# Performance work log

Hardware: AMD Instinct MI355X
Metric: run time of the kernel (lower is better)

## Reference

```python
import jax, jax.numpy as jnp
import numpy as np

DIM = 2048
K_DIM = 2048
Q_HEADS = 16
KV_HEADS = 4
HEAD_DIM = DIM // Q_HEADS  # 128
KV_DIM = HEAD_DIM * KV_HEADS  # 512
MAX_LEN = 2048
ROPE_THETA = 10000.0
ROPE_FACTOR = 8.0


def _rope_cos_sin(seq_len):
    # Faithful to generate_sin_cos_pos_emb with is_causal=True
    d = HEAD_DIM
    seq_eff = max(seq_len, MAX_LEN)
    base_adj = (ROPE_FACTOR * seq_eff / MAX_LEN - (ROPE_FACTOR - 1.0)) ** (d / (d - 2))
    adjusted_base = ROPE_THETA * base_adj
    inv_freq = 1.0 / adjusted_base ** (np.arange(0, d, 2, dtype=np.float32) / d)
    pos = np.arange(seq_len, dtype=np.float32)  # causal: no centering
    freqs = pos[:, None] * inv_freq[None, :]            # [S, d/2]
    emb = np.concatenate([freqs, freqs], axis=-1)        # [S, d]
    return jnp.asarray(np.cos(emb), jnp.float32), jnp.asarray(np.sin(emb), jnp.float32)


def _rotate_half(x):
    x1, x2 = jnp.split(x, 2, axis=-1)
    return jnp.concatenate([-x2, x1], axis=-1)


def setup_inputs() -> dict:
    key = jax.random.key(0)
    ks = jax.random.split(key, 12)
    B, S = 1, 2048
    s_in = 1.0 / np.sqrt(DIM)
    s_k = 1.0 / np.sqrt(K_DIM)
    return {
        "query": jax.random.normal(ks[0], (B, S, DIM), jnp.float32),
        "key": jax.random.normal(ks[1], (B, S, K_DIM), jnp.float32),
        "value": jax.random.normal(ks[2], (B, S, K_DIM), jnp.float32),
        "Wq": jax.random.uniform(ks[3], (DIM, DIM), jnp.float32, -s_in, s_in),
        "bq": jax.random.uniform(ks[4], (DIM,), jnp.float32, -s_in, s_in),
        "Wk": jax.random.uniform(ks[5], (KV_DIM, K_DIM), jnp.float32, -s_k, s_k),
        "bk": jax.random.uniform(ks[6], (KV_DIM,), jnp.float32, -s_k, s_k),
        "Wv": jax.random.uniform(ks[7], (KV_DIM, K_DIM), jnp.float32, -s_k, s_k),
        "bv": jax.random.uniform(ks[8], (KV_DIM,), jnp.float32, -s_k, s_k),
        "Wo": jax.random.uniform(ks[9], (DIM, DIM), jnp.float32, -s_in, s_in),
        "bo": jax.random.uniform(ks[10], (DIM,), jnp.float32, -s_in, s_in),
    }


def reference(query, key, value, Wq, bq, Wk, bk, Wv, bv, Wo, bo):
    B, S, _ = query.shape
    scale = HEAD_DIM ** -0.5

    q = query @ Wq.T + bq                                   # [B,S,DIM]
    k = key @ Wk.T + bk                                     # [B,S,KV_DIM]
    v = value @ Wv.T + bv                                   # [B,S,KV_DIM]

    q = q.reshape(B, S, Q_HEADS, HEAD_DIM)
    k = k.reshape(B, S, KV_HEADS, HEAD_DIM)
    v = v.reshape(B, S, KV_HEADS, HEAD_DIM)

    cos, sin = _rope_cos_sin(S)                              # [S,D]
    cos = cos[None, :, None, :]
    sin = sin[None, :, None, :]
    q = q * cos + _rotate_half(q) * sin
    k = k * cos + _rotate_half(k) * sin

    # [B,H,S,D]
    q = q.transpose(0, 2, 1, 3)
    k = k.transpose(0, 2, 1, 3)
    v = v.transpose(0, 2, 1, 3)

    rep = Q_HEADS // KV_HEADS
    k = jnp.repeat(k, rep, axis=1)
    v = jnp.repeat(v, rep, axis=1)

    scores = jnp.einsum('bhqd,bhkd->bhqk', q, k) * scale
    causal = jnp.tril(jnp.ones((S, S), bool))
    scores = jnp.where(causal[None, None], scores, jnp.finfo(scores.dtype).min)
    attn = jax.nn.softmax(scores, axis=-1)
    out = jnp.einsum('bhqk,bhkd->bhqd', attn, v)             # [B,H,S,D]

    out = out.transpose(0, 2, 1, 3).reshape(B, S, DIM)
    return out @ Wo.T + bo
```

## Files before the change

### kernel.cpp

```cpp
#include <hip/hip_runtime.h>
#include <stdint.h>

typedef __attribute__((ext_vector_type(8))) short short8;
typedef __attribute__((ext_vector_type(4))) float f32x4;
typedef __attribute__((ext_vector_type(4))) unsigned short u16x4;
typedef unsigned short bf16_t;

__device__ __forceinline__ bf16_t f2bf(float f) {
  union { float f; uint32_t u; } x; x.f = f;
  uint32_t r = x.u + 0x7fffu + ((x.u >> 16) & 1u);
  return (bf16_t)(r >> 16);
}

__device__ __forceinline__ void ld_g2l_16(const bf16_t* g, bf16_t* l) {
  __builtin_amdgcn_global_load_lds(
      (const __attribute__((address_space(1))) void*)g,
      (__attribute__((address_space(3))) void*)l, 16, 0, 0);
}

__global__ void rope_tab(float* __restrict__ CS, float* __restrict__ SN) {
  int idx = blockIdx.x * 256 + threadIdx.x;
  int i = idx & 63, pos = idx >> 6;
  float ang = (float)pos * exp2f((float)i * -0.2076205059f);
  CS[idx] = cosf(ang);
  SN[idx] = sinf(ang);
}

__global__ void convert_all(const float* __restrict__ s0, const float* __restrict__ s1,
                            const float* __restrict__ s2, const float* __restrict__ s3,
                            const float* __restrict__ s4, const float* __restrict__ s5,
                            const float* __restrict__ s6,
                            bf16_t* __restrict__ d0, bf16_t* __restrict__ d1,
                            bf16_t* __restrict__ d2, bf16_t* __restrict__ d3,
                            bf16_t* __restrict__ d4, bf16_t* __restrict__ d5,
                            bf16_t* __restrict__ d6) {
  int i = blockIdx.x * 256 + threadIdx.x;
  const float* src; bf16_t* dst; int off;
  if (i < 5 * 1048576) {
    int t = i >> 20; off = i & 1048575;
    if (t == 0)      { src = s0; dst = d0; }
    else if (t == 1) { src = s1; dst = d1; }
    else if (t == 2) { src = s2; dst = d2; }
    else if (t == 3) { src = s3; dst = d3; }
    else             { src = s4; dst = d4; }
  } else {
    int j = i - 5 * 1048576;
    if (j < 262144) { src = s5; dst = d5; off = j; }
    else            { src = s6; dst = d6; off = j - 262144; }
  }
  f32x4 v = *(const f32x4*)(src + (size_t)off * 4);
  u16x4 o;
  o[0] = f2bf(v[0]); o[1] = f2bf(v[1]); o[2] = f2bf(v[2]); o[3] = f2bf(v[3]);
  *(u16x4*)(dst + (size_t)off * 4) = o;
}

template <int MODE>
__device__ __forceinline__ void gemm_core(
    bf16_t* __restrict__ As, bf16_t* __restrict__ Bs,
    const bf16_t* __restrict__ A, const bf16_t* __restrict__ Bm,
    const float* __restrict__ bias, void* __restrict__ Cout,
    int N, int K, int m0, int n0,
    const float* __restrict__ CS, const float* __restrict__ SN) {
  const int tid = threadIdx.x;
  const int lane = tid & 63, quad = lane >> 4, l16 = lane & 15;
  const int wv = tid >> 6;
  const int wr = wv >> 1, wc = wv & 1;

  f32x4 acc[2][4];
  const f32x4 zf = {0.f, 0.f, 0.f, 0.f};
#pragma unroll
  for (int mi = 0; mi < 2; ++mi)
#pragma unroll
    for (int ni = 0; ni < 4; ++ni) acc[mi][ni] = zf;

  const int rA = tid >> 2, cA = (tid & 3) * 8;
  const bf16_t* Ap  = A + (size_t)(m0 + rA) * K + cA;
  const bf16_t* Bp0 = Bm + (size_t)(n0 + rA) * K + cA;
  const bf16_t* Bp1 = Bm + (size_t)(n0 + 64 + rA) * K + cA;
  bf16_t* lA  = As + tid * 8;
  bf16_t* lB0 = Bs + tid * 8;
  bf16_t* lB1 = Bs + (tid + 256) * 8;

  for (int k0 = 0; k0 < K; k0 += 32) {
    ld_g2l_16(Ap + k0, lA);
    ld_g2l_16(Bp0 + k0, lB0);
    ld_g2l_16(Bp1 + k0, lB1);
    __syncthreads();
    short8 af[2], bf[4];
#pragma unroll
    for (int mi = 0; mi < 2; ++mi)
      af[mi] = *(const short8*)(&As[(wr * 32 + mi * 16 + l16) * 32 + quad * 8]);
#pragma unroll
    for (int ni = 0; ni < 4; ++ni)
      bf[ni] = *(const short8*)(
          &Bs[(wc * 32 + (ni & 1) * 16 + (ni >> 1) * 64 + l16) * 32 + quad * 8]);
#pragma unroll
    for (int mi = 0; mi < 2; ++mi)
#pragma unroll
      for (int ni = 0; ni < 4; ++ni)
        acc[mi][ni] = __builtin_amdgcn_mfma_f32_16x16x32_bf16(
            af[mi], bf[ni], acc[mi][ni], 0, 0, 0);
    __syncthreads();
  }

  if (MODE == 0 || MODE == 2) {
#pragma unroll
    for (int mi = 0; mi < 2; ++mi)
#pragma unroll
      for (int ni = 0; ni < 4; ++ni) {
        int n = n0 + wc * 32 + (ni & 1) * 16 + (ni >> 1) * 64 + l16;
        int mbase = m0 + wr * 32 + mi * 16 + quad * 4;
        float bv = bias[n];
#pragma unroll
        for (int r = 0; r < 4; ++r) {
          float v = acc[mi][ni][r] + bv;
          int m = mbase + r;
          if (MODE == 0) ((float*)Cout)[(size_t)m * N + n] = v;
          else           ((bf16_t*)Cout)[(size_t)n * 2048 + m] = f2bf(v);
        }
      }
  } else {
    const float scale = (MODE == 3) ? 0.12751744f : 1.0f;
    bf16_t* dst = (bf16_t*)Cout;
#pragma unroll
    for (int mi = 0; mi < 2; ++mi)
#pragma unroll
      for (int r = 0; r < 4; ++r) {
        int m = m0 + wr * 32 + mi * 16 + quad * 4 + r;
#pragma unroll
        for (int ni = 0; ni < 2; ++ni) {
          int i = wc * 32 + ni * 16 + l16;
          int n_lo = n0 + i;
          float v1 = acc[mi][ni][r] + bias[n_lo];
          float v2 = acc[mi][ni + 2][r] + bias[n_lo + 64];
          float c = CS[m * 64 + i];
          float s = SN[m * 64 + i];
          float o1 = (v1 * c - v2 * s) * scale;
          float o2 = (v2 * c + v1 * s) * scale;
          dst[(size_t)m * N + n_lo] = f2bf(o1);
          dst[(size_t)m * N + n_lo + 64] = f2bf(o2);
        }
      }
  }
}

__global__ __launch_bounds__(256) void gemm_qkv(
    const bf16_t* __restrict__ qb, const bf16_t* __restrict__ kb,
    const bf16_t* __restrict__ vb, const bf16_t* __restrict__ wqb,
    const bf16_t* __restrict__ wkb, const bf16_t* __restrict__ wvb,
    const float* __restrict__ bq, const float* __restrict__ bk,
    const float* __restrict__ bv, bf16_t* __restrict__ Qr,
    bf16_t* __restrict__ Kr, bf16_t* __restrict__ Vt,
    const float* __restrict__ CS, const float* __restrict__ SN) {
  __shared__ __align__(16) bf16_t As[64 * 32];
  __shared__ __align__(16) bf16_t Bs[128 * 32];
  int bx = blockIdx.x, m0 = blockIdx.y * 64;
  if (bx < 16)
    gemm_core<3>(As, Bs, qb, wqb, bq, Qr, 2048, 2048, m0, bx * 128, CS, SN);
  else if (bx < 20)
    gemm_core<4>(As, Bs, kb, wkb, bk, Kr, 512, 2048, m0, (bx - 16) * 128, CS, SN);
  else
    gemm_core<2>(As, Bs, vb, wvb, bv, Vt, 512, 2048, m0, (bx - 20) * 128, CS, SN);
}

__global__ __launch_bounds__(256) void gemm_o(
    const bf16_t* __restrict__ Ob, const bf16_t* __restrict__ wob,
    const float* __restrict__ bo, float* __restrict__ out) {
  __shared__ __align__(16) bf16_t As[64 * 32];
  __shared__ __align__(16) bf16_t Bs[128 * 32];
  gemm_core<0>(As, Bs, Ob, wob, bo, out, 2048, 2048,
               blockIdx.y * 64, blockIdx.x * 128, nullptr, nullptr);
}

__global__ __launch_bounds__(256, 2) void attn_fwd(
    const bf16_t* __restrict__ Qr, const bf16_t* __restrict__ Kr,
    const bf16_t* __restrict__ Vt, bf16_t* __restrict__ Oo) {
  const int h = blockIdx.y;
  const int bx = blockIdx.x;
  const int qt = (h < 8) ? (31 - bx) : bx;
  const int T = qt + 1;

  const int tid = threadIdx.x;
  const int wv = tid >> 6, lane = tid & 63, quad = lane >> 4, l16 = lane & 15;
  const int q_base = qt * 64 + wv * 16;
  const int hkv = h >> 2;
  const int qg = q_base + l16;
  const int swzE = (l16 & 7) << 3;

  __shared__ __align__(16) bf16_t Ks[2][64 * 128];
  __shared__ __align__(16) bf16_t Vs[2][128 * 64];

  short8 qf[4];
  {
    const bf16_t* qp = Qr + (size_t)qg * 2048 + h * 128 + quad * 8;
#pragma unroll
    for (int kc = 0; kc < 4; ++kc) qf[kc] = *(const short8*)(qp + kc * 32);
  }

  const f32x4 zf = {0.f, 0.f, 0.f, 0.f};
  f32x4 o[8];
#pragma unroll
  for (int di = 0; di < 8; ++di) o[di] = zf;
  float l_acc = 0.f;

  auto STAGE = [&](int buf, int t) {
    const int k0 = t * 64;
    bf16_t* KB = &Ks[buf][0];
    bf16_t* VB = &Vs[buf][0];
#pragma unroll
    for (int m = 0; m < 4; ++m) {
      int rK = wv * 16 + m * 4 + (lane >> 4);
      const bf16_t* gK = Kr + (size_t)(k0 + rK) * 512 + hkv * 128
                         + (((lane & 15) ^ ((4 * (m & 1)) | quad)) << 3);
      ld_g2l_16(gK, KB + rK * 128 + ((lane & 15) << 3));
      int rV = wv * 32 + m * 8 + (lane >> 3);
      const bf16_t* gV = Vt + (size_t)(hkv * 128 + rV) * 2048 + k0
                         + (((lane & 7) ^ ((lane >> 3) & 7)) << 3);
      ld_g2l_16(gV, VB + rV * 64 + ((lane & 7) << 3));
    }
  };

  STAGE(0, 0);
  __syncthreads();
  int buf = 0;

  for (int t = 0; t < T; ++t) {
    if (t + 1 < T) STAGE(buf ^ 1, t + 1);
    const bf16_t* KB = &Ks[buf][0];
    const bf16_t* VB = &Vs[buf][0];
    const int k0 = t * 64;

    f32x4 sacc[4];
#pragma unroll
    for (int sub = 0; sub < 4; ++sub) sacc[sub] = zf;
#pragma unroll
    for (int sub = 0; sub < 4; ++sub)
#pragma unroll
      for (int kc = 0; kc < 4; ++kc) {
        short8 kf = *(const short8*)(
            &KB[(sub * 16 + l16) * 128 + ((kc * 32 + quad * 8) ^ swzE)]);
        sacc[sub] = __builtin_amdgcn_mfma_f32_16x16x32_bf16(kf, qf[kc], sacc[sub], 0, 0, 0);
      }

    const bool dg = (k0 + 63 > q_base);
    uint32_t Dw[4][2];
#pragma unroll
    for (int sub = 0; sub < 4; ++sub) {
      float pv[4];
#pragma unroll
      for (int r = 0; r < 4; ++r) {
        float e = exp2f(sacc[sub][r]);
        if (dg) {
          int kg = k0 + sub * 16 + quad * 4 + r;
          if (kg > qg) e = 0.f;
        }
        pv[r] = e;
        l_acc += e;
      }
      asm("v_cvt_pk_bf16_f32 %0, %1, %2" : "=v"(Dw[sub][0]) : "v"(pv[0]), "v"(pv[1]));
      asm("v_cvt_pk_bf16_f32 %0, %1, %2" : "=v"(Dw[sub][1]) : "v"(pv[2]), "v"(pv[3]));
    }

    const int aA = ((((quad * 2) & 3) << 4) + l16) << 2;
    const int aB = ((((quad * 2 + 1) & 3) << 4) + l16) << 2;
    const bool losel = quad < 2;
#define BPERM(a, x) ((uint32_t)__builtin_amdgcn_ds_bpermute((a), (int)(x)))
    union { uint32_t w[4]; short8 v; } U0, U1;
    {
      uint32_t t0, t1;
      t0 = BPERM(aA, Dw[0][0]); t1 = BPERM(aA, Dw[1][0]); U0.w[0] = losel ? t0 : t1;
      t0 = BPERM(aA, Dw[0][1]); t1 = BPERM(aA, Dw[1][1]); U0.w[1] = losel ? t0 : t1;
      t0 = BPERM(aB, Dw[0][0]); t1 = BPERM(aB, Dw[1][0]); U0.w[2] = losel ? t0 : t1;
      t0 = BPERM(aB, Dw[0][1]); t1 = BPERM(aB, Dw[1][1]); U0.w[3] = losel ? t0 : t1;
      t0 = BPERM(aA, Dw[2][0]); t1 = BPERM(aA, Dw[3][0]); U1.w[0] = losel ? t0 : t1;
      t0 = BPERM(aA, Dw[2][1]); t1 = BPERM(aA, Dw[3][1]); U1.w[1] = losel ? t0 : t1;
      t0 = BPERM(aB, Dw[2][0]); t1 = BPERM(aB, Dw[3][0]); U1.w[2] = losel ? t0 : t1;
      t0 = BPERM(aB, Dw[2][1]); t1 = BPERM(aB, Dw[3][1]); U1.w[3] = losel ? t0 : t1;
    }
#undef BPERM
    const short8 pf0 = U0.v, pf1 = U1.v;

#pragma unroll
    for (int di = 0; di < 8; ++di) {
      short8 vf0 = *(const short8*)(
          &VB[(di * 16 + l16) * 64 + ((quad * 8) ^ swzE)]);
      short8 vf1 = *(const short8*)(
          &VB[(di * 16 + l16) * 64 + ((quad * 8 + 32) ^ swzE)]);
      o[di] = __builtin_amdgcn_mfma_f32_16x16x32_bf16(pf0, vf0, o[di], 0, 0, 0);
      o[di] = __builtin_amdgcn_mfma_f32_16x16x32_bf16(pf1, vf1, o[di], 0, 0, 0);
    }

    __asm__ volatile("s_waitcnt vmcnt(0)" ::: "memory");
    __syncthreads();
    buf ^= 1;
  }

  float lf = l_acc;
  lf += __shfl_xor(lf, 16);
  lf += __shfl_xor(lf, 32);
  float linv[4];
#pragma unroll
  for (int r = 0; r < 4; ++r) linv[r] = 1.0f / __shfl(lf, quad * 4 + r, 64);
#pragma unroll
  for (int di = 0; di < 8; ++di)
#pragma unroll
    for (int r = 0; r < 4; ++r) {
      size_t row = q_base + quad * 4 + r;
      size_t col = h * 128 + di * 16 + l16;
      Oo[row * 2048 + col] = f2bf(o[di][r] * linv[r]);
    }
}

extern "C" void kernel_launch(void* const* d_in, const int* in_sizes, int n_in,
                              void* d_out, int out_size, void* d_ws, size_t ws_size,
                              hipStream_t stream) {
  (void)in_sizes; (void)n_in; (void)out_size; (void)ws_size;
  const float* query = (const float*)d_in[0];
  const float* key = (const float*)d_in[1];
  const float* value = (const float*)d_in[2];
  const float* Wq = (const float*)d_in[3];
  const float* bq = (const float*)d_in[4];
  const float* Wk = (const float*)d_in[5];
  const float* bk = (const float*)d_in[6];
  const float* Wv = (const float*)d_in[7];
  const float* bv = (const float*)d_in[8];
  const float* Wo = (const float*)d_in[9];
  const float* bo = (const float*)d_in[10];
  float* out = (float*)d_out;

  char* ws = (char*)d_ws;
  const size_t MB = 1024 * 1024;
  bf16_t* qb  = (bf16_t*)(ws + 0 * MB);
  bf16_t* kb  = (bf16_t*)(ws + 8 * MB);
  bf16_t* vb  = (bf16_t*)(ws + 16 * MB);
  bf16_t* wqb = (bf16_t*)(ws + 24 * MB);
  bf16_t* wkb = (bf16_t*)(ws + 32 * MB);
  bf16_t* wvb = (bf16_t*)(ws + 34 * MB);
  bf16_t* wob = (bf16_t*)(ws + 36 * MB);
  bf16_t* Qr  = (bf16_t*)(ws + 44 * MB);
  bf16_t* Kr  = (bf16_t*)(ws + 52 * MB);
  bf16_t* Vt  = (bf16_t*)(ws + 54 * MB);
  bf16_t* Ob  = (bf16_t*)(ws + 56 * MB);
  float*  CS  = (float*)(ws + 64 * MB);
  float*  SN  = (float*)(ws + 64 * MB + 512 * 1024);

  rope_tab<<<512, 256, 0, stream>>>(CS, SN);
  convert_all<<<22528, 256, 0, stream>>>(query, key, value, Wq, Wo, Wk, Wv,
                                         qb, kb, vb, wqb, wob, wkb, wvb);
  gemm_qkv<<<dim3(24, 32), 256, 0, stream>>>(qb, kb, vb, wqb, wkb, wvb,
                                             bq, bk, bv, Qr, Kr, Vt, CS, SN);
  attn_fwd<<<dim3(32, 16), 256, 0, stream>>>(Qr, Kr, Vt, Ob);
  gemm_o<<<dim3(16, 32), 256, 0, stream>>>(Ob, wob, bo, out);
}
```

Measured before the change: 273.5 us.

## Fuse all stages into one persistent megakernel with grid-wide atomic barriers

```diff
diff --git a/kernel.cpp b/kernel.cpp
--- a/kernel.cpp
+++ b/kernel.cpp
@@ -18,41 +18,24 @@
       (__attribute__((address_space(3))) void*)l, 16, 0, 0);
 }
 
-__global__ void rope_tab(float* __restrict__ CS, float* __restrict__ SN) {
-  int idx = blockIdx.x * 256 + threadIdx.x;
-  int i = idx & 63, pos = idx >> 6;
-  float ang = (float)pos * exp2f((float)i * -0.2076205059f);
-  CS[idx] = cosf(ang);
-  SN[idx] = sinf(ang);
-}
-
-__global__ void convert_all(const float* __restrict__ s0, const float* __restrict__ s1,
-                            const float* __restrict__ s2, const float* __restrict__ s3,
-                            const float* __restrict__ s4, const float* __restrict__ s5,
-                            const float* __restrict__ s6,
-                            bf16_t* __restrict__ d0, bf16_t* __restrict__ d1,
-                            bf16_t* __restrict__ d2, bf16_t* __restrict__ d3,
-                            bf16_t* __restrict__ d4, bf16_t* __restrict__ d5,
-                            bf16_t* __restrict__ d6) {
-  int i = blockIdx.x * 256 + threadIdx.x;
-  const float* src; bf16_t* dst; int off;
-  if (i < 5 * 1048576) {
-    int t = i >> 20; off = i & 1048575;
-    if (t == 0)      { src = s0; dst = d0; }
-    else if (t == 1) { src = s1; dst = d1; }
-    else if (t == 2) { src = s2; dst = d2; }
-    else if (t == 3) { src = s3; dst = d3; }
-    else             { src = s4; dst = d4; }
-  } else {
-    int j = i - 5 * 1048576;
-    if (j < 262144) { src = s5; dst = d5; off = j; }
-    else            { src = s6; dst = d6; off = j - 262144; }
-  }
-  f32x4 v = *(const f32x4*)(src + (size_t)off * 4);
-  u16x4 o;
-  o[0] = f2bf(v[0]); o[1] = f2bf(v[1]); o[2] = f2bf(v[2]); o[3] = f2bf(v[3]);
-  *(u16x4*)(dst + (size_t)off * 4) = o;
-}
+__device__ __forceinline__ void gsync(unsigned* bar, unsigned target) {
+  __syncthreads();
+  if (threadIdx.x == 0) {
+    __threadfence();
+    atomicAdd(bar, 1u);
+    while (__hip_atomic_load(bar, __ATOMIC_ACQUIRE,
+                             __HIP_MEMORY_SCOPE_AGENT) < target) {}
+    __threadfence();
+  }
+  __syncthreads();
+}
+
+struct MegaArgs {
+  const float *query, *key, *value;
+  const float *Wq, *bq, *Wk, *bk, *Wv, *bv, *Wo, *bo;
+  float* out;
+  char* ws;
+};
 
 template <int MODE>
 __device__ __forceinline__ void gemm_core(
@@ -144,39 +127,11 @@
   }
 }
 
-__global__ __launch_bounds__(256) void gemm_qkv(
-    const bf16_t* __restrict__ qb, const bf16_t* __restrict__ kb,
-    const bf16_t* __restrict__ vb, const bf16_t* __restrict__ wqb,
-    const bf16_t* __restrict__ wkb, const bf16_t* __restrict__ wvb,
-    const float* __restrict__ bq, const float* __restrict__ bk,
-    const float* __restrict__ bv, bf16_t* __restrict__ Qr,
-    bf16_t* __restrict__ Kr, bf16_t* __restrict__ Vt,
-    const float* __restrict__ CS, const float* __restrict__ SN) {
-  __shared__ __align__(16) bf16_t As[64 * 32];
-  __shared__ __align__(16) bf16_t Bs[128 * 32];
-  int bx = blockIdx.x, m0 = blockIdx.y * 64;
-  if (bx < 16)
-    gemm_core<3>(As, Bs, qb, wqb, bq, Qr, 2048, 2048, m0, bx * 128, CS, SN);
-  else if (bx < 20)
-    gemm_core<4>(As, Bs, kb, wkb, bk, Kr, 512, 2048, m0, (bx - 16) * 128, CS, SN);
-  else
-    gemm_core<2>(As, Bs, vb, wvb, bv, Vt, 512, 2048, m0, (bx - 20) * 128, CS, SN);
-}
-
-__global__ __launch_bounds__(256) void gemm_o(
-    const bf16_t* __restrict__ Ob, const bf16_t* __restrict__ wob,
-    const float* __restrict__ bo, float* __restrict__ out) {
-  __shared__ __align__(16) bf16_t As[64 * 32];
-  __shared__ __align__(16) bf16_t Bs[128 * 32];
-  gemm_core<0>(As, Bs, Ob, wob, bo, out, 2048, 2048,
-               blockIdx.y * 64, blockIdx.x * 128, nullptr, nullptr);
-}
-
-__global__ __launch_bounds__(256, 2) void attn_fwd(
-    const bf16_t* __restrict__ Qr, const bf16_t* __restrict__ Kr,
-    const bf16_t* __restrict__ Vt, bf16_t* __restrict__ Oo) {
-  const int h = blockIdx.y;
-  const int bx = blockIdx.x;
+__device__ __forceinline__ void attn_block(
+    int b, const bf16_t* __restrict__ Qr, const bf16_t* __restrict__ Kr,
+    const bf16_t* __restrict__ Vt, bf16_t* __restrict__ Oo, char* smem) {
+  const int h = b >> 5;
+  const int bx = b & 31;
   const int qt = (h < 8) ? (31 - bx) : bx;
   const int T = qt + 1;
 
@@ -187,9 +142,6 @@
   const int qg = q_base + l16;
   const int swzE = (l16 & 7) << 3;
 
-  __shared__ __align__(16) bf16_t Ks[2][64 * 128];
-  __shared__ __align__(16) bf16_t Vs[2][128 * 64];
-
   short8 qf[4];
   {
     const bf16_t* qp = Qr + (size_t)qg * 2048 + h * 128 + quad * 8;
@@ -205,8 +157,8 @@
 
   auto STAGE = [&](int buf, int t) {
     const int k0 = t * 64;
-    bf16_t* KB = &Ks[buf][0];
-    bf16_t* VB = &Vs[buf][0];
+    bf16_t* KB = (bf16_t*)(smem + buf * 16384);
+    bf16_t* VB = (bf16_t*)(smem + 32768 + buf * 16384);
 #pragma unroll
     for (int m = 0; m < 4; ++m) {
       int rK = wv * 16 + m * 4 + (lane >> 4);
@@ -226,8 +178,8 @@
 
   for (int t = 0; t < T; ++t) {
     if (t + 1 < T) STAGE(buf ^ 1, t + 1);
-    const bf16_t* KB = &Ks[buf][0];
-    const bf16_t* VB = &Vs[buf][0];
+    const bf16_t* KB = (const bf16_t*)(smem + buf * 16384);
+    const bf16_t* VB = (const bf16_t*)(smem + 32768 + buf * 16384);
     const int k0 = t * 64;
 
     f32x4 sacc[4];
@@ -311,24 +263,9 @@
     }
 }
 
-extern "C" void kernel_launch(void* const* d_in, const int* in_sizes, int n_in,
-                              void* d_out, int out_size, void* d_ws, size_t ws_size,
-                              hipStream_t stream) {
-  (void)in_sizes; (void)n_in; (void)out_size; (void)ws_size;
-  const float* query = (const float*)d_in[0];
-  const float* key = (const float*)d_in[1];
-  const float* value = (const float*)d_in[2];
-  const float* Wq = (const float*)d_in[3];
-  const float* bq = (const float*)d_in[4];
-  const float* Wk = (const float*)d_in[5];
-  const float* bk = (const float*)d_in[6];
-  const float* Wv = (const float*)d_in[7];
-  const float* bv = (const float*)d_in[8];
-  const float* Wo = (const float*)d_in[9];
-  const float* bo = (const float*)d_in[10];
-  float* out = (float*)d_out;
-
-  char* ws = (char*)d_ws;
+__global__ __launch_bounds__(256, 2) void mega(MegaArgs a) {
+  __shared__ __align__(16) char smem[65536];
+  char* ws = a.ws;
   const size_t MB = 1024 * 1024;
   bf16_t* qb  = (bf16_t*)(ws + 0 * MB);
   bf16_t* kb  = (bf16_t*)(ws + 8 * MB);
@@ -343,12 +280,83 @@
   bf16_t* Ob  = (bf16_t*)(ws + 56 * MB);
   float*  CS  = (float*)(ws + 64 * MB);
   float*  SN  = (float*)(ws + 64 * MB + 512 * 1024);
-
-  rope_tab<<<512, 256, 0, stream>>>(CS, SN);
-  convert_all<<<22528, 256, 0, stream>>>(query, key, value, Wq, Wo, Wk, Wv,
-                                         qb, kb, vb, wqb, wob, wkb, wvb);
-  gemm_qkv<<<dim3(24, 32), 256, 0, stream>>>(qb, kb, vb, wqb, wkb, wvb,
-                                             bq, bk, bv, Qr, Kr, Vt, CS, SN);
-  attn_fwd<<<dim3(32, 16), 256, 0, stream>>>(Qr, Kr, Vt, Ob);
-  gemm_o<<<dim3(16, 32), 256, 0, stream>>>(Ob, wob, bo, out);
-}
+  unsigned* bar = (unsigned*)(ws + 65 * MB);
+
+  const int b = blockIdx.x, tid = threadIdx.x;
+
+  {
+    int idx = b * 256 + tid;
+    int fi = idx & 63, pos = idx >> 6;
+    float ang = (float)pos * exp2f((float)fi * -0.2076205059f);
+    CS[idx] = cosf(ang);
+    SN[idx] = sinf(ang);
+    for (int i = idx; i < 5767168; i += 131072) {
+      const float* src; bf16_t* dst; int off;
+      if (i < 5242880) {
+        int t = i >> 20; off = i & 1048575;
+        if (t == 0)      { src = a.query; dst = qb; }
+        else if (t == 1) { src = a.key;   dst = kb; }
+        else if (t == 2) { src = a.value; dst = vb; }
+        else if (t == 3) { src = a.Wq;    dst = wqb; }
+        else             { src = a.Wo;    dst = wob; }
+      } else {
+        int j = i - 5242880;
+        if (j < 262144) { src = a.Wk; dst = wkb; off = j; }
+        else            { src = a.Wv; dst = wvb; off = j - 262144; }
+      }
+      f32x4 v = *(const f32x4*)(src + (size_t)off * 4);
+      u16x4 o4;
+      o4[0] = f2bf(v[0]); o4[1] = f2bf(v[1]); o4[2] = f2bf(v[2]); o4[3] = f2bf(v[3]);
+      *(u16x4*)(dst + (size_t)off * 4) = o4;
+    }
+  }
+  gsync(&bar[0], 512);
+
+  {
+    bf16_t* As = (bf16_t*)smem;
+    bf16_t* Bs = (bf16_t*)(smem + 4096);
+    int j = b;
+    for (int rnd = 0; rnd < 2; ++rnd) {
+      int bx = j % 24, m0 = (j / 24) * 64;
+      if (bx < 16)
+        gemm_core<3>(As, Bs, qb, wqb, a.bq, Qr, 2048, 2048, m0, bx * 128, CS, SN);
+      else if (bx < 20)
+        gemm_core<4>(As, Bs, kb, wkb, a.bk, Kr, 512, 2048, m0, (bx - 16) * 128, CS, SN);
+      else
+        gemm_core<2>(As, Bs, vb, wvb, a.bv, Vt, 512, 2048, m0, (bx - 20) * 128, CS, SN);
+      if ((b & 1) != 0 || rnd == 1) break;
+      j = 512 + (b >> 1);
+      __syncthreads();
+    }
+  }
+  gsync(&bar[1], 512);
+
+  attn_block(b, Qr, Kr, Vt, Ob, smem);
+  gsync(&bar[2], 512);
+
+  {
+    bf16_t* As = (bf16_t*)smem;
+    bf16_t* Bs = (bf16_t*)(smem + 4096);
+    gemm_core<0>(As, Bs, Ob, wob, a.bo, a.out, 2048, 2048,
+                 (b >> 4) * 64, (b & 15) * 128, nullptr, nullptr);
+  }
+}
+
+extern "C" void kernel_launch(void* const* d_in, const int* in_sizes, int n_in,
+                              void* d_out, int out_size, void* d_ws, size_t ws_size,
+                              hipStream_t stream) {
+  (void)in_sizes; (void)n_in; (void)out_size; (void)ws_size;
+  MegaArgs a;
+  a.query = (const float*)d_in[0];
+  a.key   = (const float*)d_in[1];
+  a.value = (const float*)d_in[2];
+  a.Wq = (const float*)d_in[3];  a.bq = (const float*)d_in[4];
+  a.Wk = (const float*)d_in[5];  a.bk = (const float*)d_in[6];
+  a.Wv = (const float*)d_in[7];  a.bv = (const float*)d_in[8];
+  a.Wo = (const float*)d_in[9];  a.bo = (const float*)d_in[10];
+  a.out = (float*)d_out;
+  a.ws = (char*)d_ws;
+
+  hipMemsetAsync(a.ws + 65 * 1024 * 1024, 0, 256, stream);
+  mega<<<dim3(512), dim3(256), 0, stream>>>(a);
+}
```

Result: slower. 578.4 us (+111.5%).

## Load V fragments directly into registers and fold RoPE table into convert

Applied to the files above, without the earlier changes.

```diff
diff --git a/kernel.cpp b/kernel.cpp
--- a/kernel.cpp
+++ b/kernel.cpp
@@ -16,14 +16,6 @@
   __builtin_amdgcn_global_load_lds(
       (const __attribute__((address_space(1))) void*)g,
       (__attribute__((address_space(3))) void*)l, 16, 0, 0);
-}
-
-__global__ void rope_tab(float* __restrict__ CS, float* __restrict__ SN) {
-  int idx = blockIdx.x * 256 + threadIdx.x;
-  int i = idx & 63, pos = idx >> 6;
-  float ang = (float)pos * exp2f((float)i * -0.2076205059f);
-  CS[idx] = cosf(ang);
-  SN[idx] = sinf(ang);
 }
 
 __global__ void convert_all(const float* __restrict__ s0, const float* __restrict__ s1,
@@ -33,8 +25,15 @@
                             bf16_t* __restrict__ d0, bf16_t* __restrict__ d1,
                             bf16_t* __restrict__ d2, bf16_t* __restrict__ d3,
                             bf16_t* __restrict__ d4, bf16_t* __restrict__ d5,
-                            bf16_t* __restrict__ d6) {
+                            bf16_t* __restrict__ d6,
+                            float* __restrict__ CS, float* __restrict__ SN) {
   int i = blockIdx.x * 256 + threadIdx.x;
+  if (i < 131072) {
+    int fi = i & 63, pos = i >> 6;
+    float ang = (float)pos * exp2f((float)fi * -0.2076205059f);
+    CS[i] = cosf(ang);
+    SN[i] = sinf(ang);
+  }
   const float* src; bf16_t* dst; int off;
   if (i < 5 * 1048576) {
     int t = i >> 20; off = i & 1048575;
@@ -188,7 +187,6 @@
   const int swzE = (l16 & 7) << 3;
 
   __shared__ __align__(16) bf16_t Ks[2][64 * 128];
-  __shared__ __align__(16) bf16_t Vs[2][128 * 64];
 
   short8 qf[4];
   {
@@ -197,37 +195,43 @@
     for (int kc = 0; kc < 4; ++kc) qf[kc] = *(const short8*)(qp + kc * 32);
   }
 
+  const bf16_t* Vb = Vt + ((size_t)hkv * 128 + l16) * 2048 + quad * 8;
+
   const f32x4 zf = {0.f, 0.f, 0.f, 0.f};
   f32x4 o[8];
 #pragma unroll
   for (int di = 0; di < 8; ++di) o[di] = zf;
   float l_acc = 0.f;
 
-  auto STAGE = [&](int buf, int t) {
+  auto STAGE_K = [&](int buf, int t) {
     const int k0 = t * 64;
     bf16_t* KB = &Ks[buf][0];
-    bf16_t* VB = &Vs[buf][0];
 #pragma unroll
     for (int m = 0; m < 4; ++m) {
       int rK = wv * 16 + m * 4 + (lane >> 4);
       const bf16_t* gK = Kr + (size_t)(k0 + rK) * 512 + hkv * 128
                          + (((lane & 15) ^ ((4 * (m & 1)) | quad)) << 3);
       ld_g2l_16(gK, KB + rK * 128 + ((lane & 15) << 3));
-      int rV = wv * 32 + m * 8 + (lane >> 3);
-      const bf16_t* gV = Vt + (size_t)(hkv * 128 + rV) * 2048 + k0
-                         + (((lane & 7) ^ ((lane >> 3) & 7)) << 3);
-      ld_g2l_16(gV, VB + rV * 64 + ((lane & 7) << 3));
     }
   };
-
-  STAGE(0, 0);
-  __syncthreads();
-  int buf = 0;
-
-  for (int t = 0; t < T; ++t) {
-    if (t + 1 < T) STAGE(buf ^ 1, t + 1);
-    const bf16_t* KB = &Ks[buf][0];
-    const bf16_t* VB = &Vs[buf][0];
+  auto LOADV = [&](short8 (&vf)[8][2], int t) {
+    const int k0 = t * 64;
+#pragma unroll
+    for (int di = 0; di < 8; ++di) {
+      vf[di][0] = *(const short8*)(Vb + (size_t)(di * 16) * 2048 + k0);
+      vf[di][1] = *(const short8*)(Vb + (size_t)(di * 16) * 2048 + k0 + 32);
+    }
+  };
+
+  short8 vA[8][2], vB[8][2];
+
+  auto ITER = [&](int t, short8 (&vcur)[8][2], short8 (&vnxt)[8][2]) {
+    const int p = t & 1;
+    if (t + 1 < T) {
+      STAGE_K(p ^ 1, t + 1);
+      LOADV(vnxt, t + 1);
+    }
+    const bf16_t* KB = &Ks[p][0];
     const int k0 = t * 64;
 
     f32x4 sacc[4];
@@ -282,17 +286,22 @@
 
 #pragma unroll
     for (int di = 0; di < 8; ++di) {
-      short8 vf0 = *(const short8*)(
-          &VB[(di * 16 + l16) * 64 + ((quad * 8) ^ swzE)]);
-      short8 vf1 = *(const short8*)(
-          &VB[(di * 16 + l16) * 64 + ((quad * 8 + 32) ^ swzE)]);
-      o[di] = __builtin_amdgcn_mfma_f32_16x16x32_bf16(pf0, vf0, o[di], 0, 0, 0);
-      o[di] = __builtin_amdgcn_mfma_f32_16x16x32_bf16(pf1, vf1, o[di], 0, 0, 0);
+      o[di] = __builtin_amdgcn_mfma_f32_16x16x32_bf16(pf0, vcur[di][0], o[di], 0, 0, 0);
+      o[di] = __builtin_amdgcn_mfma_f32_16x16x32_bf16(pf1, vcur[di][1], o[di], 0, 0, 0);
     }
 
     __asm__ volatile("s_waitcnt vmcnt(0)" ::: "memory");
     __syncthreads();
-    buf ^= 1;
+  };
+
+  STAGE_K(0, 0);
+  LOADV(vA, 0);
+  __syncthreads();
+
+  int t = 0;
+  for (;;) {
+    ITER(t, vA, vB); if (++t >= T) break;
+    ITER(t, vB, vA); if (++t >= T) break;
   }
 
   float lf = l_acc;
@@ -344,9 +353,8 @@
   float*  CS  = (float*)(ws + 64 * MB);
   float*  SN  = (float*)(ws + 64 * MB + 512 * 1024);
 
-  rope_tab<<<512, 256, 0, stream>>>(CS, SN);
   convert_all<<<22528, 256, 0, stream>>>(query, key, value, Wq, Wo, Wk, Wv,
-                                         qb, kb, vb, wqb, wob, wkb, wvb);
+                                         qb, kb, vb, wqb, wob, wkb, wvb, CS, SN);
   gemm_qkv<<<dim3(24, 32), 256, 0, stream>>>(qb, kb, vb, wqb, wkb, wvb,
                                              bq, bk, bv, Qr, Kr, Vt, CS, SN);
   attn_fwd<<<dim3(32, 16), 256, 0, stream>>>(Qr, Kr, Vt, Ob);
```

Result: slower. 420.6 us (+53.8%).

## Double-buffer GEMM LDS staging and fold RoPE table into convert kernel

Applied to the files above, without the earlier changes.

```diff
diff --git a/kernel.cpp b/kernel.cpp
--- a/kernel.cpp
+++ b/kernel.cpp
@@ -16,14 +16,6 @@
   __builtin_amdgcn_global_load_lds(
       (const __attribute__((address_space(1))) void*)g,
       (__attribute__((address_space(3))) void*)l, 16, 0, 0);
-}
-
-__global__ void rope_tab(float* __restrict__ CS, float* __restrict__ SN) {
-  int idx = blockIdx.x * 256 + threadIdx.x;
-  int i = idx & 63, pos = idx >> 6;
-  float ang = (float)pos * exp2f((float)i * -0.2076205059f);
-  CS[idx] = cosf(ang);
-  SN[idx] = sinf(ang);
 }
 
 __global__ void convert_all(const float* __restrict__ s0, const float* __restrict__ s1,
@@ -33,8 +25,15 @@
                             bf16_t* __restrict__ d0, bf16_t* __restrict__ d1,
                             bf16_t* __restrict__ d2, bf16_t* __restrict__ d3,
                             bf16_t* __restrict__ d4, bf16_t* __restrict__ d5,
-                            bf16_t* __restrict__ d6) {
+                            bf16_t* __restrict__ d6,
+                            float* __restrict__ CS, float* __restrict__ SN) {
   int i = blockIdx.x * 256 + threadIdx.x;
+  if (i < 131072) {
+    int fi = i & 63, pos = i >> 6;
+    float ang = (float)pos * exp2f((float)fi * -0.2076205059f);
+    CS[i] = cosf(ang);
+    SN[i] = sinf(ang);
+  }
   const float* src; bf16_t* dst; int off;
   if (i < 5 * 1048576) {
     int t = i >> 20; off = i & 1048575;
@@ -77,30 +76,38 @@
   const bf16_t* Ap  = A + (size_t)(m0 + rA) * K + cA;
   const bf16_t* Bp0 = Bm + (size_t)(n0 + rA) * K + cA;
   const bf16_t* Bp1 = Bm + (size_t)(n0 + 64 + rA) * K + cA;
-  bf16_t* lA  = As + tid * 8;
-  bf16_t* lB0 = Bs + tid * 8;
-  bf16_t* lB1 = Bs + (tid + 256) * 8;
+
+  auto STAGE = [&](int buf, int k0) {
+    ld_g2l_16(Ap + k0, As + buf * 2048 + tid * 8);
+    ld_g2l_16(Bp0 + k0, Bs + buf * 4096 + tid * 8);
+    ld_g2l_16(Bp1 + k0, Bs + buf * 4096 + (tid + 256) * 8);
+  };
+
+  STAGE(0, 0);
+  __syncthreads();
+  int buf = 0;
 
   for (int k0 = 0; k0 < K; k0 += 32) {
-    ld_g2l_16(Ap + k0, lA);
-    ld_g2l_16(Bp0 + k0, lB0);
-    ld_g2l_16(Bp1 + k0, lB1);
-    __syncthreads();
+    if (k0 + 32 < K) STAGE(buf ^ 1, k0 + 32);
+    const bf16_t* Ab = As + buf * 2048;
+    const bf16_t* Bb = Bs + buf * 4096;
     short8 af[2], bf[4];
 #pragma unroll
     for (int mi = 0; mi < 2; ++mi)
-      af[mi] = *(const short8*)(&As[(wr * 32 + mi * 16 + l16) * 32 + quad * 8]);
+      af[mi] = *(const short8*)(&Ab[(wr * 32 + mi * 16 + l16) * 32 + quad * 8]);
 #pragma unroll
     for (int ni = 0; ni < 4; ++ni)
       bf[ni] = *(const short8*)(
-          &Bs[(wc * 32 + (ni & 1) * 16 + (ni >> 1) * 64 + l16) * 32 + quad * 8]);
+          &Bb[(wc * 32 + (ni & 1) * 16 + (ni >> 1) * 64 + l16) * 32 + quad * 8]);
 #pragma unroll
     for (int mi = 0; mi < 2; ++mi)
 #pragma unroll
       for (int ni = 0; ni < 4; ++ni)
         acc[mi][ni] = __builtin_amdgcn_mfma_f32_16x16x32_bf16(
             af[mi], bf[ni], acc[mi][ni], 0, 0, 0);
+    __asm__ volatile("s_waitcnt vmcnt(0)" ::: "memory");
     __syncthreads();
+    buf ^= 1;
   }
 
   if (MODE == 0 || MODE == 2) {
@@ -152,8 +159,8 @@
     const float* __restrict__ bv, bf16_t* __restrict__ Qr,
     bf16_t* __restrict__ Kr, bf16_t* __restrict__ Vt,
     const float* __restrict__ CS, const float* __restrict__ SN) {
-  __shared__ __align__(16) bf16_t As[64 * 32];
-  __shared__ __align__(16) bf16_t Bs[128 * 32];
+  __shared__ __align__(16) bf16_t As[2 * 64 * 32];
+  __shared__ __align__(16) bf16_t Bs[2 * 128 * 32];
   int bx = blockIdx.x, m0 = blockIdx.y * 64;
   if (bx < 16)
     gemm_core<3>(As, Bs, qb, wqb, bq, Qr, 2048, 2048, m0, bx * 128, CS, SN);
@@ -166,8 +173,8 @@
 __global__ __launch_bounds__(256) void gemm_o(
     const bf16_t* __restrict__ Ob, const bf16_t* __restrict__ wob,
     const float* __restrict__ bo, float* __restrict__ out) {
-  __shared__ __align__(16) bf16_t As[64 * 32];
-  __shared__ __align__(16) bf16_t Bs[128 * 32];
+  __shared__ __align__(16) bf16_t As[2 * 64 * 32];
+  __shared__ __align__(16) bf16_t Bs[2 * 128 * 32];
   gemm_core<0>(As, Bs, Ob, wob, bo, out, 2048, 2048,
                blockIdx.y * 64, blockIdx.x * 128, nullptr, nullptr);
 }
@@ -344,9 +351,8 @@
   float*  CS  = (float*)(ws + 64 * MB);
   float*  SN  = (float*)(ws + 64 * MB + 512 * 1024);
 
-  rope_tab<<<512, 256, 0, stream>>>(CS, SN);
   convert_all<<<22528, 256, 0, stream>>>(query, key, value, Wq, Wo, Wk, Wv,
-                                         qb, kb, vb, wqb, wob, wkb, wvb);
+                                         qb, kb, vb, wqb, wob, wkb, wvb, CS, SN);
   gemm_qkv<<<dim3(24, 32), 256, 0, stream>>>(qb, kb, vb, wqb, wkb, wvb,
                                              bq, bk, bv, Qr, Kr, Vt, CS, SN);
   attn_fwd<<<dim3(32, 16), 256, 0, stream>>>(Qr, Kr, Vt, Ob);
```

After: 276.8 us. Within noise of the previous version (+1.2%).
